# Kernel optimization log

Hardware: AMD Instinct MI355X
Metric: run time of the kernel (lower is better)

Reference implementation:

```python
import jax, jax.numpy as jnp
import numpy as np

BASE_T = 0.07
ALPHA = 0.5
EPS = 1e-12  # torch F.normalize eps


def _l2_normalize(x):
    norm = jnp.linalg.norm(x, axis=1, keepdims=True)
    return x / jnp.maximum(norm, EPS)


def setup_inputs() -> dict:
    key = jax.random.key(0)
    k1, k2, k3 = jax.random.split(key, 3)
    B, D, H, W = 4096, 512, 16, 16
    return {
        "emb1": jax.random.normal(k1, (B, D), dtype=jnp.float32),
        "emb2": jax.random.normal(k2, (B, D), dtype=jnp.float32),
        "attention_map": jax.random.uniform(k3, (B, H, W), dtype=jnp.float32),
    }


def reference(emb1, emb2, attention_map):
    B = emb1.shape[0]
    e1 = _l2_normalize(emb1)
    e2 = _l2_normalize(emb2)

    att = attention_map.mean(axis=(1, 2))                     # [B]
    temp = (BASE_T * (1.0 + ALPHA * att))[:, None]            # [B, 1]

    x = jnp.concatenate([e1, e2], axis=0)                     # [2B, D]
    x_swap = jnp.concatenate([e2, e1], axis=0)                # [2B, D]
    temp_cat = jnp.concatenate([temp, temp], axis=0)          # [2B, 1]

    sim = jnp.matmul(x, x.T) / temp_cat                       # [2B, 2B]
    pos_sim = jnp.sum(x * x_swap, axis=1) / temp_cat[:, 0]    # [2B]

    diag = jnp.eye(2 * B, dtype=bool)
    sim = jnp.where(diag, -jnp.inf, sim)                      # exp(-inf) = 0

    denominator = jnp.exp(sim).sum(axis=1)                    # [2B]
    loss = -jnp.log(jnp.exp(pos_sim) / denominator)
    return loss.mean()
```

## Files before the change

kernel.cpp:

```cpp
#include <hip/hip_runtime.h>
#include <hip/hip_bf16.h>
#include <math.h>

#define B_ROWS 4096
#define D_DIM 512
#define TWO_B 8192
#define HW_N 256
#define BASE_T 0.07f
#define ALPHA_C 0.5f
#define LOG2E 1.44269504088896340736f

typedef float v4f __attribute__((ext_vector_type(4)));

__device__ __forceinline__ float fast_exp2(float x) {
#if __has_builtin(__builtin_amdgcn_exp2f)
    return __builtin_amdgcn_exp2f(x);
#else
    return exp2f(x);
#endif
}

__global__ __launch_bounds__(256) void prep_kernel(
    const float* __restrict__ emb1, const float* __restrict__ emb2,
    const float* __restrict__ att, unsigned short* __restrict__ X8,
    float* __restrict__ inv_temp, float* __restrict__ pos,
    float* __restrict__ out)
{
    const int b = blockIdx.x;
    const int t = threadIdx.x;
    const float2 a1 = ((const float2*)(emb1 + (size_t)b * D_DIM))[t];
    const float2 a2 = ((const float2*)(emb2 + (size_t)b * D_DIM))[t];
    float av = att[(size_t)b * HW_N + t];
    float s1  = a1.x * a1.x + a1.y * a1.y;
    float s2  = a2.x * a2.x + a2.y * a2.y;
    float s12 = a1.x * a2.x + a1.y * a2.y;
    #pragma unroll
    for (int m = 1; m < 64; m <<= 1) {
        s1  += __shfl_xor(s1, m, 64);
        s2  += __shfl_xor(s2, m, 64);
        s12 += __shfl_xor(s12, m, 64);
        av  += __shfl_xor(av, m, 64);
    }
    __shared__ float red[4][4];
    const int w = t >> 6, lane = t & 63;
    if (lane == 0) { red[w][0] = s1; red[w][1] = s2; red[w][2] = s12; red[w][3] = av; }
    __syncthreads();
    const float T1  = red[0][0] + red[1][0] + red[2][0] + red[3][0];
    const float T2  = red[0][1] + red[1][1] + red[2][1] + red[3][1];
    const float T12 = red[0][2] + red[1][2] + red[2][2] + red[3][2];
    const float Ta  = red[0][3] + red[1][3] + red[2][3] + red[3][3];
    const float i1 = 1.0f / fmaxf(sqrtf(T1), 1e-12f);
    const float i2 = 1.0f / fmaxf(sqrtf(T2), 1e-12f);
    const float it = 1.0f / (BASE_T * (1.0f + ALPHA_C * (Ta * (1.0f / 256.0f))));
    const int p1 = __builtin_amdgcn_cvt_pk_fp8_f32(a1.x * i1, a1.y * i1, 0, false);
    const int p2 = __builtin_amdgcn_cvt_pk_fp8_f32(a2.x * i2, a2.y * i2, 0, false);
    X8[(size_t)b * 256 + t]            = (unsigned short)(p1 & 0xffff);
    X8[(size_t)(b + B_ROWS) * 256 + t] = (unsigned short)(p2 & 0xffff);
    if (t == 0) {
        inv_temp[b] = it * LOG2E;
        inv_temp[b + B_ROWS] = it * LOG2E;
        pos[b] = (T12 * i1 * i2) * it;
        if (b == 0) out[0] = 0.0f;
    }
}

__device__ __forceinline__ void gload_lds16(const void* g, void* s) {
    __builtin_amdgcn_global_load_lds(
        (const __attribute__((address_space(1))) unsigned int*)g,
        (__attribute__((address_space(3))) unsigned int*)s,
        16, 0, 0);
}

__global__ __launch_bounds__(256, 3) void gram_kernel(
    const unsigned char* __restrict__ X8,
    const float* __restrict__ inv_temp,
    float* __restrict__ partial)
{
    const int bid = (blockIdx.x & 7) * 260 + (blockIdx.x >> 3);
    int rb = (int)((129.0f - sqrtf(129.0f * 129.0f - 8.0f * (float)bid)) * 0.5f);
    rb = rb < 0 ? 0 : (rb > 63 ? 63 : rb);
    while (rb > 0 && (rb * (129 - rb)) / 2 > bid) rb--;
    while (rb < 63 && ((rb + 1) * (129 - (rb + 1))) / 2 <= bid) rb++;
    const int cb = rb + (bid - (rb * (129 - rb)) / 2);

    __shared__ unsigned char smA[3][8192];
    __shared__ unsigned char smB[3][8192];

    const int rowBase = rb * 128;
    const int colBase = cb * 128;

    const int tid  = threadIdx.x;
    const int w    = tid >> 6;
    const int lane = tid & 63;
    const int quad = lane >> 4;
    const int t    = lane & 15;
    const int wm   = w >> 1;
    const int wn   = w & 1;

    const int lr = lane >> 2;
    const int su = lane & 3;

    const unsigned char* Arow0 = X8 + (size_t)rowBase * D_DIM;
    const unsigned char* Brow0 = X8 + (size_t)colBase * D_DIM;

    v4f acc[4][4];
    #pragma unroll
    for (int a = 0; a < 4; a++)
        #pragma unroll
        for (int b2 = 0; b2 < 4; b2++)
            acc[a][b2] = v4f{0.0f, 0.0f, 0.0f, 0.0f};

    const int hb = (t >> 1) & 3;
    const int aBase = (wm * 64 + t) * 64;
    const int bBase = (wn * 64 + t) * 64;

#define STAGE(BUF, KK) do {                                                   \
    _Pragma("unroll")                                                         \
    for (int j = 0; j < 2; j++) {                                             \
        const int g = w * 2 + j;                \
        const int r = g * 16 + lr;                                            \
        const int gc = su ^ ((r >> 1) & 3);  \
        gload_lds16(Arow0 + (size_t)r * D_DIM + (KK) + gc * 16,               \
                    &smA[BUF][g * 1024]);                                     \
        gload_lds16(Brow0 + (size_t)r * D_DIM + (KK) + gc * 16,               \
                    &smB[BUF][g * 1024]);                                     \
    }                                                                         \
} while (0)

#define COMPUTE(BUF) do {                                                     \
    _Pragma("unroll")                                                         \
    for (int s = 0; s < 2; s++) {                                             \
        const int pu = (s * 2 + (quad >> 1)) ^ hb;                            \
        const int off = pu * 16 + (quad & 1) * 8;                             \
        long aF[4], bF[4];                                                    \
        _Pragma("unroll")                                                     \
        for (int mi = 0; mi < 4; mi++)                                        \
            aF[mi] = *(const long*)&smA[BUF][aBase + mi * 1024 + off];        \
        _Pragma("unroll")                                                     \
        for (int ni = 0; ni < 4; ni++)                                        \
            bF[ni] = *(const long*)&smB[BUF][bBase + ni * 1024 + off];        \
        _Pragma("unroll")                                                     \
        for (int mi = 0; mi < 4; mi++)                                        \
            _Pragma("unroll")                                                 \
            for (int ni = 0; ni < 4; ni++)                                    \
                acc[mi][ni] = __builtin_amdgcn_mfma_f32_16x16x32_fp8_fp8(     \
                    aF[mi], bF[ni], acc[mi][ni], 0, 0, 0);                    \
    }                                                                         \
} while (0)

#define SYNC_N(N) do {                                                        \
    asm volatile("s_waitcnt vmcnt(" #N ")" ::: "memory");                     \
    __builtin_amdgcn_s_barrier();                                             \
    asm volatile("" ::: "memory");                                            \
} while (0)

    STAGE(0, 0);
    STAGE(1, 64);
    SYNC_N(4);

    STAGE(2, 128);  COMPUTE(0);  SYNC_N(4);
    STAGE(0, 192);  COMPUTE(1);  SYNC_N(4);
    STAGE(1, 256);  COMPUTE(2);  SYNC_N(4);
    STAGE(2, 320);  COMPUTE(0);  SYNC_N(4);
    STAGE(0, 384);  COMPUTE(1);  SYNC_N(4);
    STAGE(1, 448);  COMPUTE(2);  SYNC_N(4);
    COMPUTE(0);     SYNC_N(0);
    COMPUTE(1);

#undef STAGE
#undef COMPUTE
#undef SYNC_N

    v4f itv[4];
    #pragma unroll
    for (int mi = 0; mi < 4; mi++)
        itv[mi] = *(const v4f*)&inv_temp[rowBase + wm * 64 + mi * 16 + quad * 4];

    float* prow = partial + (size_t)(cb * 2 + wn) * TWO_B;
    #pragma unroll
    for (int mi = 0; mi < 4; mi++) {
        #pragma unroll
        for (int r = 0; r < 4; r++) {
            const int i = rowBase + wm * 64 + mi * 16 + quad * 4 + r;
            const float it = itv[mi][r];
            float s = 0.0f;
            #pragma unroll
            for (int ni = 0; ni < 4; ni++) {
                const int j = colBase + wn * 64 + ni * 16 + t;
                const float v = fast_exp2(acc[mi][ni][r] * it);
                s += (i == j) ? 0.0f : v;
            }
            s += __shfl_xor(s, 1, 64);
            s += __shfl_xor(s, 2, 64);
            s += __shfl_xor(s, 4, 64);
            s += __shfl_xor(s, 8, 64);
            if (t == 0) prow[i] = s;
        }
    }

    if (rb != cb) {
        float itj[4];
        float cs[4] = {0.0f, 0.0f, 0.0f, 0.0f};
        #pragma unroll
        for (int ni = 0; ni < 4; ni++)
            itj[ni] = inv_temp[colBase + wn * 64 + ni * 16 + t];
        #pragma unroll
        for (int mi = 0; mi < 4; mi++)
            #pragma unroll
            for (int r = 0; r < 4; r++)
                #pragma unroll
                for (int ni = 0; ni < 4; ni++)
                    cs[ni] += fast_exp2(acc[mi][ni][r] * itj[ni]);
        float* pcol = partial + (size_t)(rb * 2 + wm) * TWO_B;
        #pragma unroll
        for (int ni = 0; ni < 4; ni++) {
            cs[ni] += __shfl_xor(cs[ni], 16, 64);
            cs[ni] += __shfl_xor(cs[ni], 32, 64);
            if (quad == 0) pcol[colBase + wn * 64 + ni * 16 + t] = cs[ni];
        }
    }
}

__global__ __launch_bounds__(256) void finish1(
    const float* __restrict__ partial, const float* __restrict__ pos,
    float* __restrict__ out)
{
    const int i = blockIdx.x * 256 + threadIdx.x;
    float d = 0.0f;
    #pragma unroll 8
    for (int s = 0; s < 128; s++) d += partial[(size_t)s * TWO_B + i];
    float li = logf(d) - pos[i & (B_ROWS - 1)];
    #pragma unroll
    for (int m = 1; m < 64; m <<= 1) li += __shfl_xor(li, m, 64);
    __shared__ float red[4];
    const int w = threadIdx.x >> 6, lane = threadIdx.x & 63;
    if (lane == 0) red[w] = li;
    __syncthreads();
    if (threadIdx.x == 0)
        atomicAdd(out, (red[0] + red[1] + red[2] + red[3]) * (1.0f / 8192.0f));
}

extern "C" void kernel_launch(void* const* d_in, const int* in_sizes, int n_in,
                              void* d_out, int out_size, void* d_ws, size_t ws_size,
                              hipStream_t stream) {
    const float* emb1 = (const float*)d_in[0];
    const float* emb2 = (const float*)d_in[1];
    const float* att  = (const float*)d_in[2];
    float* out = (float*)d_out;

    char* ws = (char*)d_ws;
    unsigned short* X8 = (unsigned short*)ws;
    float* inv_temp    = (float*)(ws + 4194304);
    float* pos         = (float*)(ws + 4194304 + 32768);
    float* partial     = (float*)(ws + 4194304 + 32768 + 16384);

    prep_kernel<<<B_ROWS, 256, 0, stream>>>(emb1, emb2, att, X8, inv_temp, pos, out);
    gram_kernel<<<2080, 256, 0, stream>>>((const unsigned char*)X8, inv_temp, partial);
    finish1<<<TWO_B / 256, 256, 0, stream>>>(partial, pos, out);
}
```

Measured before the change: 121.3 us.

## Process two triangular tiles per block, prefetching the second tile during the first epilogue

Each gram block now computes two consecutive upper-triangular 128x128 tiles instead of one, halving the grid to 1040 blocks. The first K-loads of the second tile are issued while the first tile's last compute and exp epilogue run, hiding that load latency. The LDS pipeline moves from triple to double buffering with __syncthreads, s_setprio is raised around the MFMA sections, and the launch_bounds occupancy hint is removed. This trades wave-level parallelism and load balance for less per-block prologue and epilogue cost, and may change register allocation and occupancy.

```diff
diff --git a/kernel.cpp b/kernel.cpp
--- a/kernel.cpp
+++ b/kernel.cpp
@@ -71,105 +71,22 @@
         16, 0, 0);
 }
 
-__global__ __launch_bounds__(256, 3) void gram_kernel(
-    const unsigned char* __restrict__ X8,
-    const float* __restrict__ inv_temp,
-    float* __restrict__ partial)
-{
-    const int bid = (blockIdx.x & 7) * 260 + (blockIdx.x >> 3);
-    int rb = (int)((129.0f - sqrtf(129.0f * 129.0f - 8.0f * (float)bid)) * 0.5f);
-    rb = rb < 0 ? 0 : (rb > 63 ? 63 : rb);
-    while (rb > 0 && (rb * (129 - rb)) / 2 > bid) rb--;
-    while (rb < 63 && ((rb + 1) * (129 - (rb + 1))) / 2 <= bid) rb++;
-    const int cb = rb + (bid - (rb * (129 - rb)) / 2);
-
-    __shared__ unsigned char smA[3][8192];
-    __shared__ unsigned char smB[3][8192];
-
+__device__ __forceinline__ void tri_decode(int bid, int& rb, int& cb) {
+    int r = (int)((129.0f - sqrtf(129.0f * 129.0f - 8.0f * (float)bid)) * 0.5f);
+    r = r < 0 ? 0 : (r > 63 ? 63 : r);
+    while (r > 0 && (r * (129 - r)) / 2 > bid) r--;
+    while (r < 63 && ((r + 1) * (129 - (r + 1))) / 2 <= bid) r++;
+    rb = r;
+    cb = r + (bid - (r * (129 - r)) / 2);
+}
+
+__device__ __forceinline__ void do_epilogue(
+    const v4f (&acc)[4][4], const float* __restrict__ inv_temp,
+    float* __restrict__ partial, int rb, int cb,
+    int wm, int wn, int quad, int t)
+{
     const int rowBase = rb * 128;
     const int colBase = cb * 128;
-
-    const int tid  = threadIdx.x;
-    const int w    = tid >> 6;
-    const int lane = tid & 63;
-    const int quad = lane >> 4;
-    const int t    = lane & 15;
-    const int wm   = w >> 1;
-    const int wn   = w & 1;
-
-    const int lr = lane >> 2;
-    const int su = lane & 3;
-
-    const unsigned char* Arow0 = X8 + (size_t)rowBase * D_DIM;
-    const unsigned char* Brow0 = X8 + (size_t)colBase * D_DIM;
-
-    v4f acc[4][4];
-    #pragma unroll
-    for (int a = 0; a < 4; a++)
-        #pragma unroll
-        for (int b2 = 0; b2 < 4; b2++)
-            acc[a][b2] = v4f{0.0f, 0.0f, 0.0f, 0.0f};
-
-    const int hb = (t >> 1) & 3;
-    const int aBase = (wm * 64 + t) * 64;
-    const int bBase = (wn * 64 + t) * 64;
-
-#define STAGE(BUF, KK) do {                                                   \
-    _Pragma("unroll")                                                         \
-    for (int j = 0; j < 2; j++) {                                             \
-        const int g = w * 2 + j;                \
-        const int r = g * 16 + lr;                                            \
-        const int gc = su ^ ((r >> 1) & 3);  \
-        gload_lds16(Arow0 + (size_t)r * D_DIM + (KK) + gc * 16,               \
-                    &smA[BUF][g * 1024]);                                     \
-        gload_lds16(Brow0 + (size_t)r * D_DIM + (KK) + gc * 16,               \
-                    &smB[BUF][g * 1024]);                                     \
-    }                                                                         \
-} while (0)
-
-#define COMPUTE(BUF) do {                                                     \
-    _Pragma("unroll")                                                         \
-    for (int s = 0; s < 2; s++) {                                             \
-        const int pu = (s * 2 + (quad >> 1)) ^ hb;                            \
-        const int off = pu * 16 + (quad & 1) * 8;                             \
-        long aF[4], bF[4];                                                    \
-        _Pragma("unroll")                                                     \
-        for (int mi = 0; mi < 4; mi++)                                        \
-            aF[mi] = *(const long*)&smA[BUF][aBase + mi * 1024 + off];        \
-        _Pragma("unroll")                                                     \
-        for (int ni = 0; ni < 4; ni++)                                        \
-            bF[ni] = *(const long*)&smB[BUF][bBase + ni * 1024 + off];        \
-        _Pragma("unroll")                                                     \
-        for (int mi = 0; mi < 4; mi++)                                        \
-            _Pragma("unroll")                                                 \
-            for (int ni = 0; ni < 4; ni++)                                    \
-                acc[mi][ni] = __builtin_amdgcn_mfma_f32_16x16x32_fp8_fp8(     \
-                    aF[mi], bF[ni], acc[mi][ni], 0, 0, 0);                    \
-    }                                                                         \
-} while (0)
-
-#define SYNC_N(N) do {                                                        \
-    asm volatile("s_waitcnt vmcnt(" #N ")" ::: "memory");                     \
-    __builtin_amdgcn_s_barrier();                                             \
-    asm volatile("" ::: "memory");                                            \
-} while (0)
-
-    STAGE(0, 0);
-    STAGE(1, 64);
-    SYNC_N(4);
-
-    STAGE(2, 128);  COMPUTE(0);  SYNC_N(4);
-    STAGE(0, 192);  COMPUTE(1);  SYNC_N(4);
-    STAGE(1, 256);  COMPUTE(2);  SYNC_N(4);
-    STAGE(2, 320);  COMPUTE(0);  SYNC_N(4);
-    STAGE(0, 384);  COMPUTE(1);  SYNC_N(4);
-    STAGE(1, 448);  COMPUTE(2);  SYNC_N(4);
-    COMPUTE(0);     SYNC_N(0);
-    COMPUTE(1);
-
-#undef STAGE
-#undef COMPUTE
-#undef SYNC_N
 
     v4f itv[4];
     #pragma unroll
@@ -221,7 +138,119 @@
     }
 }
 
-__global__ __launch_bounds__(256) void finish1(
+__global__ void gram_kernel(
+    const unsigned char* __restrict__ X8,
+    const float* __restrict__ inv_temp,
+    float* __restrict__ partial)
+{
+    const int id = (blockIdx.x & 7) * 130 + (blockIdx.x >> 3);
+    int rb0, cb0, rb1, cb1;
+    tri_decode(2 * id,     rb0, cb0);
+    tri_decode(2 * id + 1, rb1, cb1);
+
+    __shared__ unsigned char smA[2][8192];
+    __shared__ unsigned char smB[2][8192];
+
+    const int tid  = threadIdx.x;
+    const int w    = tid >> 6;
+    const int lane = tid & 63;
+    const int quad = lane >> 4;
+    const int t    = lane & 15;
+    const int wm   = w >> 1;
+    const int wn   = w & 1;
+
+    const int lr = lane >> 2;
+    const int su = lane & 3;
+
+    const unsigned char* A0 = X8 + (size_t)(rb0 * 128) * D_DIM;
+    const unsigned char* B0 = X8 + (size_t)(cb0 * 128) * D_DIM;
+    const unsigned char* A1 = X8 + (size_t)(rb1 * 128) * D_DIM;
+    const unsigned char* B1 = X8 + (size_t)(cb1 * 128) * D_DIM;
+
+    v4f acc[4][4];
+    #pragma unroll
+    for (int a = 0; a < 4; a++)
+        #pragma unroll
+        for (int b2 = 0; b2 < 4; b2++)
+            acc[a][b2] = v4f{0.0f, 0.0f, 0.0f, 0.0f};
+
+    const int hb = (t >> 1) & 3;
+    const int aBase = (wm * 64 + t) * 64;
+    const int bBase = (wn * 64 + t) * 64;
+
+#define STAGE(BUF, AP, BP, KK) do {                                           \
+    _Pragma("unroll")                                                         \
+    for (int j = 0; j < 2; j++) {                                             \
+        const int g = w * 2 + j;                \
+        const int r = g * 16 + lr;                                            \
+        const int gc = su ^ ((r >> 1) & 3);  \
+        gload_lds16((AP) + (size_t)r * D_DIM + (KK) + gc * 16,                \
+                    &smA[BUF][g * 1024]);                                     \
+        gload_lds16((BP) + (size_t)r * D_DIM + (KK) + gc * 16,                \
+                    &smB[BUF][g * 1024]);                                     \
+    }                                                                         \
+} while (0)
+
+#define COMPUTE(CUR) do {                                                     \
+    __builtin_amdgcn_s_setprio(1);                                            \
+    _Pragma("unroll")                                                         \
+    for (int s = 0; s < 2; s++) {                                             \
+        const int pu = (s * 2 + (quad >> 1)) ^ hb;                            \
+        const int off = pu * 16 + (quad & 1) * 8;                             \
+        long aF[4], bF[4];                                                    \
+        _Pragma("unroll")                                                     \
+        for (int mi = 0; mi < 4; mi++)                                        \
+            aF[mi] = *(const long*)&smA[CUR][aBase + mi * 1024 + off];        \
+        _Pragma("unroll")                                                     \
+        for (int ni = 0; ni < 4; ni++)                                        \
+            bF[ni] = *(const long*)&smB[CUR][bBase + ni * 1024 + off];        \
+        _Pragma("unroll")                                                     \
+        for (int mi = 0; mi < 4; mi++)                                        \
+            _Pragma("unroll")                                                 \
+            for (int ni = 0; ni < 4; ni++)                                    \
+                acc[mi][ni] = __builtin_amdgcn_mfma_f32_16x16x32_fp8_fp8(     \
+                    aF[mi], bF[ni], acc[mi][ni], 0, 0, 0);                    \
+    }                                                                         \
+    __builtin_amdgcn_s_setprio(0);                                            \
+} while (0)
+
+    STAGE(0, A0, B0, 0);
+    __syncthreads();
+
+    #pragma unroll
+    for (int p = 0; p < 8; p++) {
+        const int cur = p & 1;
+        if (p < 7) {
+            STAGE(cur ^ 1, A0, B0, (p + 1) * 64);
+        } else {
+            STAGE(cur ^ 1, A1, B1, 0);
+        }
+        COMPUTE(cur);
+        if (p == 7) {
+            do_epilogue(acc, inv_temp, partial, rb0, cb0, wm, wn, quad, t);
+            #pragma unroll
+            for (int a = 0; a < 4; a++)
+                #pragma unroll
+                for (int b2 = 0; b2 < 4; b2++)
+                    acc[a][b2] = v4f{0.0f, 0.0f, 0.0f, 0.0f};
+        }
+        __syncthreads();
+    }
+
+    #pragma unroll
+    for (int p = 0; p < 8; p++) {
+        const int cur = p & 1;
+        if (p < 7) STAGE(cur ^ 1, A1, B1, (p + 1) * 64);
+        COMPUTE(cur);
+        if (p < 7) __syncthreads();
+    }
+    do_epilogue(acc, inv_temp, partial, rb1, cb1, wm, wn, quad, t);
+
+#undef STAGE
+#undef COMPUTE
+}
+
+__global__ __launch_bounds__(256) void finishk(
     const float* __restrict__ partial, const float* __restrict__ pos,
     float* __restrict__ out)
 {
@@ -255,6 +284,6 @@
     float* partial     = (float*)(ws + 4194304 + 32768 + 16384);
 
     prep_kernel<<<B_ROWS, 256, 0, stream>>>(emb1, emb2, att, X8, inv_temp, pos, out);
-    gram_kernel<<<2080, 256, 0, stream>>>((const unsigned char*)X8, inv_temp, partial);
-    finish1<<<TWO_B / 256, 256, 0, stream>>>(partial, pos, out);
-}
+    gram_kernel<<<1040, 256, 0, stream>>>((const unsigned char*)X8, inv_temp, partial);
+    finishk<<<TWO_B / 256, 256, 0, stream>>>(partial, pos, out);
+}
```

Result: slower. 130.4 us (+7.5%).
